# Performance work log

Measured on AMD Instinct MI355X. Metric: run time of the kernel, lower is better.

Reference implementation:

```python
import jax, jax.numpy as jnp
import numpy as np

B = 65536      # graphs per batch
NPG = 8        # nodes per graph (row_cluster has 8 entries)
N = B * NPG    # total nodes
P = 3 * B      # pooled nodes (3 row-clusters per graph)


def setup_inputs() -> dict:
    key = jax.random.key(0)
    ks = jax.random.split(key, 10)
    # per-graph edge template (undirected -> both directions); rows: {0,1,2},{3,4,5},{6,7}
    pairs = np.array([(0, 1), (1, 2), (0, 3), (3, 4), (4, 5), (3, 6), (6, 7), (2, 5), (5, 7), (1, 7)], dtype=np.int64)
    und = np.concatenate([pairs, pairs[:, ::-1]], axis=0)              # [20,2]
    off = (np.arange(B, dtype=np.int64) * NPG)[:, None, None]
    ei = (und[None] + off).reshape(-1, 2).T                            # [2, 20B]
    # pooled edges = avg_pool's coalesced cluster graph: triangle on 3 clusters per graph
    ppairs = np.array([(0, 1), (1, 2), (0, 2)], dtype=np.int64)
    pund = np.concatenate([ppairs, ppairs[:, ::-1]], axis=0)           # [6,2]
    poff = (np.arange(B, dtype=np.int64) * 3)[:, None, None]
    ei2 = (pund[None] + poff).reshape(-1, 2).T                         # [2, 6B]
    # consecutive-relabelled cluster assignment (PyG: 3*batch + [1,1,1,2,2,2,3,3] -> 0..3B-1)
    cluster = np.tile(np.array([0, 0, 0, 1, 1, 1, 2, 2], dtype=np.int64), B) + np.repeat(np.arange(B, dtype=np.int64) * 3, NPG)
    batch2 = np.arange(P, dtype=np.int64) // 3

    def lin(k, fan_in, fan_out):
        kw, kb = jax.random.split(k)
        s = 1.0 / np.sqrt(fan_in)
        W = jax.random.uniform(kw, (fan_in, fan_out), minval=-s, maxval=s, dtype=jnp.float32)
        b = jax.random.uniform(kb, (fan_out,), minval=-s, maxval=s, dtype=jnp.float32)
        return W, b

    W1, b1 = lin(ks[0], 336, 100)
    W2, b2 = lin(ks[1], 100, 100)
    W3, b3 = lin(ks[2], 100, 100)
    W4, b4 = lin(ks[3], 100, 100)
    W5, b5 = lin(ks[4], 100, 100)
    L1w, L1b = lin(ks[5], 100, 100)
    L2w, L2b = lin(ks[6], 100, 100)
    L3w, L3b = lin(ks[7], 100, 29)
    x = jax.random.normal(ks[8], (N, 336), dtype=jnp.float32)
    return dict(x=x, edge_index=jnp.asarray(ei), edge_index2=jnp.asarray(ei2),
                cluster=jnp.asarray(cluster), batch2=jnp.asarray(batch2),
                W1=W1, b1=b1, W2=W2, b2=b2, W3=W3, b3=b3, W4=W4, b4=b4, W5=W5, b5=b5,
                L1w=L1w, L1b=L1b, L2w=L2w, L2b=L2b, L3w=L3w, L3b=L3b)


def gcn(x, ei, W, b, n):
    # PyG GCNConv: x' = D^{-1/2}(A+I)D^{-1/2} (x W) + b
    h = x @ W
    loop = jnp.arange(n)
    s = jnp.concatenate([ei[0], loop])
    d = jnp.concatenate([ei[1], loop])
    deg = jax.ops.segment_sum(jnp.ones(s.shape[0], h.dtype), d, num_segments=n)
    dinv = jax.lax.rsqrt(deg)  # deg >= 1 because of self-loops
    norm = dinv[s] * dinv[d]
    return jax.ops.segment_sum(h[s] * norm[:, None], d, num_segments=n) + b


def reference(x, edge_index, edge_index2, cluster, batch2,
              W1, b1, W2, b2, W3, b3, W4, b4, W5, b5,
              L1w, L1b, L2w, L2b, L3w, L3b):
    h = jax.nn.relu(gcn(x, edge_index, W1, b1, N))
    h = jax.nn.relu(gcn(h, edge_index, W2, b2, N))
    h = jax.nn.relu(gcn(h, edge_index, W3, b3, N))
    # avg_pool: mean node features per cluster -> [P, 100]
    cnt = jax.ops.segment_sum(jnp.ones(N, h.dtype), cluster, num_segments=P)
    hp = jax.ops.segment_sum(h, cluster, num_segments=P) / cnt[:, None]
    hp = jax.nn.relu(gcn(hp, edge_index2, W4, b4, P))
    hp = jax.nn.relu(gcn(hp, edge_index2, W5, b5, P))
    # global_mean_pool over pooled-graph batch -> [B, 100]
    cnt2 = jax.ops.segment_sum(jnp.ones(P, hp.dtype), batch2, num_segments=B)
    g = jax.ops.segment_sum(hp, batch2, num_segments=B) / cnt2[:, None]
    g = jax.nn.relu(g @ L1w + L1b)
    g = jax.nn.relu(g @ L2w + L2b)
    return g @ L3w + L3b
```

## Files before the change

kernel.cpp:

```cpp
#include <hip/hip_runtime.h>


typedef __bf16 bf16_t;
typedef bf16_t bf16x8 __attribute__((ext_vector_type(8)));
typedef unsigned short u16x8 __attribute__((ext_vector_type(8)));
typedef float f32x4 __attribute__((ext_vector_type(4)));

#define C_ 0.28867513459481287f
#define T_ (1.0f/3.0f)
#define Q_ 0.25f

#define OFF_W1  0
#define OFF_W2  39424
#define OFF_W3  53760
#define OFF_W4  68096
#define OFF_W5  82432
#define OFF_L1W 96768
#define OFF_L2W 111104
#define OFF_L3W 125440
#define M_OFF_BYTES 262144

__device__ __forceinline__ unsigned short f2bf(float f) {
  return __builtin_bit_cast(unsigned short, (__bf16)f);
}
__device__ __forceinline__ float bf2f(unsigned short h) {
  unsigned u = ((unsigned)h) << 16;
  return __builtin_bit_cast(float, u);
}

__global__ __launch_bounds__(256) void prep_w(
    const float* __restrict__ W1, const float* __restrict__ W2,
    const float* __restrict__ W3, const float* __restrict__ W4,
    const float* __restrict__ W5, const float* __restrict__ L1w,
    const float* __restrict__ L2w, const float* __restrict__ L3w,
    unsigned short* __restrict__ ws)
{
  const int bid = blockIdx.x;
  int m, ct;
  if (bid < 7)       { m = 0; ct = bid; }
  else if (bid < 49) { m = 1 + (bid - 7) / 7; ct = (bid - 7) % 7; }
  else               { m = 7; ct = bid - 49; }
  const float* W; int K, NC, KSF; int off;
  switch (m) {
    case 0:  W = W1;  K = 336; NC = 100; KSF = 11; off = OFF_W1;  break;
    case 1:  W = W2;  K = 100; NC = 100; KSF = 4;  off = OFF_W2;  break;
    case 2:  W = W3;  K = 100; NC = 100; KSF = 4;  off = OFF_W3;  break;
    case 3:  W = W4;  K = 100; NC = 100; KSF = 4;  off = OFF_W4;  break;
    case 4:  W = W5;  K = 100; NC = 100; KSF = 4;  off = OFF_W5;  break;
    case 5:  W = L1w; K = 100; NC = 100; KSF = 4;  off = OFF_L1W; break;
    case 6:  W = L2w; K = 100; NC = 100; KSF = 4;  off = OFF_L2W; break;
    default: W = L3w; K = 100; NC = 29;  KSF = 4;  off = OFF_L3W; break;
  }
  for (int task = threadIdx.x; task < KSF * 64; task += 256) {
    const int ks = task >> 6, lane = task & 63;
    const int col = ct * 16 + (lane & 15);
    u16x8 o;
#pragma unroll
    for (int j = 0; j < 8; ++j) {
      const int k = ks * 32 + (lane >> 4) * 8 + j;
      const float v = (k < K && col < NC) ? W[(size_t)k * NC + col] : 0.f;
      o[j] = f2bf(v);
    }
    *(u16x8*)(ws + off + (size_t)(ct * KSF + ks) * 512 + (size_t)lane * 8) = o;
  }
}

#define MFMA1(ACC, AH, BH)                                                     \
  ACC = __builtin_amdgcn_mfma_f32_16x16x32_bf16(                               \
      __builtin_bit_cast(bf16x8, AH), __builtin_bit_cast(bf16x8, BH), ACC,     \
      0, 0, 0)

#define MFMA2S(ACC, AH, AL, BH)                                                \
  do {                                                                         \
    MFMA1(ACC, AH, BH);                                                        \
    MFMA1(ACC, AL, BH);                                                        \
  } while (0)

#define LOADB(MOFF, KSF_, CT, KS, BH)                                          \
  BH = *(const u16x8*)(ws + (MOFF) +                                           \
                       (size_t)((CT) * (KSF_) + (KS)) * 512 + lane8)

#define STORE_H(R, Cc, V)                                                      \
  do {                                                                         \
    const unsigned short hb_ = f2bf(V);                                        \
    const int pb_ = (R) * 256 + ((((Cc) * 2)) ^ (((R) & 7) << 4));             \
    *(unsigned short*)(Ahi + pb_) = hb_;                                       \
  } while (0)

#define DENSE_KLOOP(MOFF)                                                      \
  do {                                                                         \
    _Pragma("unroll")                                                          \
    for (int rt = 0; rt < 2; ++rt)                                             \
      _Pragma("unroll")                                                        \
      for (int ct = 0; ct < 7; ++ct) acc[rt][ct] = (f32x4){0.f, 0.f, 0.f, 0.f};\
    _Pragma("unroll 1")                                                        \
    for (int ks = 0; ks < 4; ++ks) {                                           \
      u16x8 ah[2];                                                             \
      _Pragma("unroll")                                                        \
      for (int rt = 0; rt < 2; ++rt) {                                         \
        const int row = w32 + rt * 16 + l15;                                   \
        const int pb = row * 256 + ((ks * 64 + q16) ^ ((row & 7) << 4));       \
        ah[rt] = *(const u16x8*)(Ahi + pb);                                    \
      }                                                                        \
      _Pragma("unroll")                                                        \
      for (int ct = 0; ct < 7; ++ct) {                                         \
        u16x8 bh;                                                              \
        LOADB(MOFF, 4, ct, ks, bh);                                            \
        MFMA1(acc[0][ct], ah[0], bh);                                          \
        MFMA1(acc[1][ct], ah[1], bh);                                          \
      }                                                                        \
    }                                                                          \
  } while (0)

#define EPI_MIX(BV)                                                            \
  do {                                                                         \
    _Pragma("unroll")                                                          \
    for (int rt = 0; rt < 2; ++rt) {                                           \
      _Pragma("unroll")                                                        \
      for (int ct = 0; ct < 7; ++ct) {                                         \
        const float v0 = acc[rt][ct][0], v1 = acc[rt][ct][1];                  \
        const float v2 = acc[rt][ct][2], v3 = acc[rt][ct][3];                  \
        const float u0 = __shfl_xor(v0, 16), u1 = __shfl_xor(v1, 16);          \
        const float u2 = __shfl_xor(v2, 16), u3 = __shfl_xor(v3, 16);          \
        float o0, o1, o2, o3;                                                  \
        if (!p1) {            \
          o0 = T_ * v0 + C_ * (v1 + v3);                                       \
          o1 = C_ * (v0 + v2) + Q_ * (v1 + u3);                                \
          o2 = T_ * v2 + C_ * (v1 + u1);                                       \
          o3 = Q_ * v3 + C_ * (v0 + u0 + u2);                                  \
        } else {              \
          o0 = T_ * v0 + C_ * (u3 + v1);                                       \
          o1 = Q_ * (v1 + v3) + C_ * (v0 + u2);                                \
          o2 = T_ * v2 + C_ * (u3 + v3);                                       \
          o3 = Q_ * (v3 + v1 + u1) + C_ * v2;                                  \
        }                                                                      \
        const int col = ct * 16 + l15;                                         \
        const float bv = BV[ct];                                               \
        float h0 = fmaxf(o0 + bv, 0.f), h1 = fmaxf(o1 + bv, 0.f);              \
        float h2 = fmaxf(o2 + bv, 0.f), h3 = fmaxf(o3 + bv, 0.f);              \
        if (col >= 100) { h0 = h1 = h2 = h3 = 0.f; }                           \
        const int rb = w32 + rt * 16 + 4 * q;                                  \
        STORE_H(rb + 0, col, h0); STORE_H(rb + 1, col, h1);                    \
        STORE_H(rb + 2, col, h2); STORE_H(rb + 3, col, h3);                    \
      }                                                                        \
    }                                                                          \
  } while (0)

__global__ __launch_bounds__(256, 3)
void rownet_node(const float* __restrict__ x,
                 const unsigned short* __restrict__ ws,
                 unsigned char* __restrict__ mws,
                 const float* __restrict__ b1, const float* __restrict__ b2,
                 const float* __restrict__ b3)
{
  __shared__ __align__(16) unsigned char smem[32768];
  unsigned char* const Ahi = smem;

  const int tid  = threadIdx.x;
  const int w    = tid >> 6;
  const int lane = tid & 63;
  const int l15  = lane & 15;
  const int q    = lane >> 4;
  const int q16  = q * 16;
  const int p1   = q & 1;
  const int lane8 = lane * 8;
  const int w32  = w * 32;
  const int g0   = blockIdx.x * 16;
  const int n0   = blockIdx.x * 128;

  float bv1[7], bv2[7], bv3[7];
#pragma unroll
  for (int ct = 0; ct < 7; ++ct) {
    const int col = ct * 16 + l15;
    const bool ok = (col < 100);
    bv1[ct] = ok ? b1[col] : 0.f;
    bv2[ct] = ok ? b2[col] : 0.f;
    bv3[ct] = ok ? b3[col] : 0.f;
  }

  f32x4 acc[2][7];

  {
    const float* const xb =
        x + (size_t)(n0 + w32 + l15) * 336 + q * 8;
    const bool qlow = (q < 2);
#pragma unroll
    for (int rt = 0; rt < 2; ++rt)
#pragma unroll
      for (int ct = 0; ct < 7; ++ct) acc[rt][ct] = (f32x4){0.f, 0.f, 0.f, 0.f};

#pragma unroll 1
    for (int ks = 0; ks < 11; ++ks) {
      u16x8 ah[2], al[2];
#pragma unroll
      for (int rt = 0; rt < 2; ++rt) {
        float4 p0, p1v;
        if (ks < 10 || qlow) {
          const float* xr = xb + (size_t)rt * (16 * 336) + ks * 32;
          p0  = *(const float4*)xr;
          p1v = *(const float4*)(xr + 4);
        } else {
          p0 = make_float4(0.f, 0.f, 0.f, 0.f);
          p1v = p0;
        }
        const float v[8] = {p0.x, p0.y, p0.z, p0.w, p1v.x, p1v.y, p1v.z, p1v.w};
#pragma unroll
        for (int j = 0; j < 8; ++j) {
          const unsigned short hb = f2bf(v[j]);
          ah[rt][j] = hb;
          al[rt][j] = f2bf(v[j] - bf2f(hb));
        }
      }
#pragma unroll
      for (int ct = 0; ct < 7; ++ct) {
        u16x8 bh;
        LOADB(OFF_W1, 11, ct, ks, bh);
#pragma unroll
        for (int rt = 0; rt < 2; ++rt)
          MFMA2S(acc[rt][ct], ah[rt], al[rt], bh);
      }
    }
  }
  {
    const int row = w32 + (lane & 31);
    const int half = lane >> 5;
    const int pb = row * 256 + ((224 + 16 * half) ^ ((row & 7) << 4));
    *(u16x8*)(Ahi + pb) = (u16x8){0, 0, 0, 0, 0, 0, 0, 0};
  }

  EPI_MIX(bv1);

  DENSE_KLOOP(OFF_W2);  EPI_MIX(bv2);
  DENSE_KLOOP(OFF_W3);

#pragma unroll
  for (int rt = 0; rt < 2; ++rt) {
#pragma unroll
    for (int ct = 0; ct < 7; ++ct) {
      const float v0 = acc[rt][ct][0], v1 = acc[rt][ct][1];
      const float v2 = acc[rt][ct][2], v3 = acc[rt][ct][3];
      const float u0 = __shfl_xor(v0, 16), u1 = __shfl_xor(v1, 16);
      const float u2 = __shfl_xor(v2, 16), u3 = __shfl_xor(v3, 16);
      float o0, o1, o2, o3;
      if (!p1) {
        o0 = T_ * v0 + C_ * (v1 + v3);
        o1 = C_ * (v0 + v2) + Q_ * (v1 + u3);
        o2 = T_ * v2 + C_ * (v1 + u1);
        o3 = Q_ * v3 + C_ * (v0 + u0 + u2);
      } else {
        o0 = T_ * v0 + C_ * (u3 + v1);
        o1 = Q_ * (v1 + v3) + C_ * (v0 + u2);
        o2 = T_ * v2 + C_ * (u3 + v3);
        o3 = Q_ * (v3 + v1 + u1) + C_ * v2;
      }
      const int col = ct * 16 + l15;
      const float bv = bv3[ct];
      float h0 = fmaxf(o0 + bv, 0.f), h1 = fmaxf(o1 + bv, 0.f);
      float h2 = fmaxf(o2 + bv, 0.f), h3 = fmaxf(o3 + bv, 0.f);
      if (col >= 100) { h0 = h1 = h2 = h3 = 0.f; }
      float pp = p1 ? ((h0 + h1) * (1.f/9.f) + (h2 + h3) * (1.f/6.f))
                    : ((h0 + h1 + h2 + h3) * (1.f/9.f));
      pp += __shfl_xor(pp, 16);
      if (!p1 && col < 100) {
        const int g_abs = g0 + 4 * w + 2 * rt + (q >> 1);
        const int blk2 = g_abs >> 7, r2 = g_abs & 127;
        const size_t byte = (size_t)blk2 * 32768 + r2 * 256
                          + ((col * 2) ^ ((r2 & 7) << 4));
        *(unsigned short*)(mws + byte) = f2bf(pp);
      }
    }
  }
}

#define EPI_PLAIN(BOFF)                                                        \
  do {                                                                         \
    _Pragma("unroll")                                                          \
    for (int rt = 0; rt < 2; ++rt) {                                           \
      _Pragma("unroll")                                                        \
      for (int ct = 0; ct < 7; ++ct) {                                         \
        const int col = ct * 16 + l15;                                         \
        const float bv = bs[(BOFF) + col];                                     \
        _Pragma("unroll")                                                      \
        for (int i = 0; i < 4; ++i) {                                          \
          float hv = fmaxf(acc[rt][ct][i] + bv, 0.f);                          \
          if (col >= 100) hv = 0.f;                                            \
          STORE_H(w32 + rt * 16 + 4 * q + i, col, hv);                         \
        }                                                                      \
      }                                                                        \
    }                                                                          \
  } while (0)

__global__ __launch_bounds__(256, 3)
void rownet_tail(const unsigned short* __restrict__ ws,
                 const unsigned char* __restrict__ mws,
                 const float* __restrict__ b4, const float* __restrict__ b5,
                 const float* __restrict__ L1b, const float* __restrict__ L2b,
                 const float* __restrict__ L3b,
                 float* __restrict__ out)
{
  __shared__ __align__(16) unsigned char smem[34496];
  unsigned char* const Ahi = smem;
  float* const bs = (float*)(smem + 32768);

  const int tid  = threadIdx.x;
  const int w    = tid >> 6;
  const int lane = tid & 63;
  const int l15  = lane & 15;
  const int q    = lane >> 4;
  const int q16  = q * 16;
  const int lane8 = lane * 8;
  const int w32  = w * 32;

  {
    const unsigned char* src = mws + (size_t)blockIdx.x * 32768;
#pragma unroll
    for (int it = 0; it < 8; ++it) {
      const int off = (it * 256 + tid) * 16;
      *(u16x8*)(Ahi + off) = *(const u16x8*)(src + off);
    }
  }
  if (tid < 100) {
    bs[      tid] = b4[tid];
    bs[100 + tid] = b5[tid];
    bs[200 + tid] = L1b[tid];
    bs[300 + tid] = L2b[tid];
  }
  if (tid < 29) bs[400 + tid] = L3b[tid];
  __syncthreads();

  f32x4 acc[2][7];
  DENSE_KLOOP(OFF_W4);  EPI_PLAIN(0);
  DENSE_KLOOP(OFF_W5);  EPI_PLAIN(100);
  DENSE_KLOOP(OFF_L1W); EPI_PLAIN(200);
  DENSE_KLOOP(OFF_L2W); EPI_PLAIN(300);

  {
    f32x4 c[2][2];
#pragma unroll
    for (int rt = 0; rt < 2; ++rt)
#pragma unroll
      for (int ct = 0; ct < 2; ++ct) c[rt][ct] = (f32x4){0.f, 0.f, 0.f, 0.f};
#pragma unroll
    for (int ks = 0; ks < 4; ++ks) {
      u16x8 ah[2];
#pragma unroll
      for (int rt = 0; rt < 2; ++rt) {
        const int row = w32 + rt * 16 + l15;
        const int pb = row * 256 + ((ks * 64 + q16) ^ ((row & 7) << 4));
        ah[rt] = *(const u16x8*)(Ahi + pb);
      }
#pragma unroll
      for (int ct = 0; ct < 2; ++ct) {
        u16x8 bh;
        LOADB(OFF_L3W, 4, ct, ks, bh);
        MFMA1(c[0][ct], ah[0], bh);
        MFMA1(c[1][ct], ah[1], bh);
      }
    }
    const size_t gbase = (size_t)blockIdx.x * 128;
#pragma unroll
    for (int rt = 0; rt < 2; ++rt)
#pragma unroll
      for (int ct = 0; ct < 2; ++ct) {
        const int col = ct * 16 + l15;
        if (col < 29) {
#pragma unroll
          for (int i = 0; i < 4; ++i) {
            const int row = w32 + rt * 16 + 4 * q + i;
            out[(gbase + row) * 29 + col] = c[rt][ct][i] + bs[400 + col];
          }
        }
      }
  }
}

extern "C" void kernel_launch(void* const* d_in, const int* in_sizes, int n_in,
                              void* d_out, int out_size, void* d_ws, size_t ws_size,
                              hipStream_t stream) {
  (void)in_sizes; (void)n_in; (void)out_size; (void)ws_size;
  const float* x   = (const float*)d_in[0];
  const float* W1  = (const float*)d_in[5];
  const float* b1  = (const float*)d_in[6];
  const float* W2  = (const float*)d_in[7];
  const float* b2  = (const float*)d_in[8];
  const float* W3  = (const float*)d_in[9];
  const float* b3  = (const float*)d_in[10];
  const float* W4  = (const float*)d_in[11];
  const float* b4  = (const float*)d_in[12];
  const float* W5  = (const float*)d_in[13];
  const float* b5  = (const float*)d_in[14];
  const float* L1w = (const float*)d_in[15];
  const float* L1b = (const float*)d_in[16];
  const float* L2w = (const float*)d_in[17];
  const float* L2b = (const float*)d_in[18];
  const float* L3w = (const float*)d_in[19];
  const float* L3b = (const float*)d_in[20];
  unsigned short* ws = (unsigned short*)d_ws;
  unsigned char* mws = (unsigned char*)d_ws + M_OFF_BYTES;

  prep_w<<<51, 256, 0, stream>>>(W1, W2, W3, W4, W5, L1w, L2w, L3w, ws);
  rownet_node<<<4096, 256, 0, stream>>>(x, ws, mws, b1, b2, b3);
  rownet_tail<<<512, 256, 0, stream>>>(ws, mws, b4, b5, L1b, L2b, L3b,
                                       (float*)d_out);
}
```

Measured before the change: 299.5 us.

## Process 64 rows per wave with 2-wave blocks in node kernel

The node kernel now runs 128-thread blocks where each wave handles 64 rows (4 row tiles) instead of 32, so each B-fragment load of the weights feeds four MFMAs instead of two. This halves weight-load traffic per MFMA and the number of waves per block. The cost is twice the accumulator registers (acc[4][7]) and a lower launch-bounds occupancy target, with fewer waves available to hide latency. The old 2-row-tile loop macro is kept for the tail kernel.

New measurement: 353.9 us. +18.2%, slower.

```diff
diff --git a/kernel.cpp b/kernel.cpp
--- a/kernel.cpp
+++ b/kernel.cpp
@@ -87,18 +87,18 @@
     *(unsigned short*)(Ahi + pb_) = hb_;                                       \
   } while (0)
 
-#define DENSE_KLOOP(MOFF)                                                      \
+#define DENSE_KLOOP4(MOFF)                                                     \
   do {                                                                         \
     _Pragma("unroll")                                                          \
-    for (int rt = 0; rt < 2; ++rt)                                             \
+    for (int rt = 0; rt < 4; ++rt)                                             \
       _Pragma("unroll")                                                        \
       for (int ct = 0; ct < 7; ++ct) acc[rt][ct] = (f32x4){0.f, 0.f, 0.f, 0.f};\
     _Pragma("unroll 1")                                                        \
     for (int ks = 0; ks < 4; ++ks) {                                           \
-      u16x8 ah[2];                                                             \
-      _Pragma("unroll")                                                        \
-      for (int rt = 0; rt < 2; ++rt) {                                         \
-        const int row = w32 + rt * 16 + l15;                                   \
+      u16x8 ah[4];                                                             \
+      _Pragma("unroll")                                                        \
+      for (int rt = 0; rt < 4; ++rt) {                                         \
+        const int row = w64 + rt * 16 + l15;                                   \
         const int pb = row * 256 + ((ks * 64 + q16) ^ ((row & 7) << 4));       \
         ah[rt] = *(const u16x8*)(Ahi + pb);                                    \
       }                                                                        \
@@ -108,14 +108,16 @@
         LOADB(MOFF, 4, ct, ks, bh);                                            \
         MFMA1(acc[0][ct], ah[0], bh);                                          \
         MFMA1(acc[1][ct], ah[1], bh);                                          \
+        MFMA1(acc[2][ct], ah[2], bh);                                          \
+        MFMA1(acc[3][ct], ah[3], bh);                                          \
       }                                                                        \
     }                                                                          \
   } while (0)
 
-#define EPI_MIX(BV)                                                            \
+#define EPI_MIX4(BV)                                                           \
   do {                                                                         \
     _Pragma("unroll")                                                          \
-    for (int rt = 0; rt < 2; ++rt) {                                           \
+    for (int rt = 0; rt < 4; ++rt) {                                           \
       _Pragma("unroll")                                                        \
       for (int ct = 0; ct < 7; ++ct) {                                         \
         const float v0 = acc[rt][ct][0], v1 = acc[rt][ct][1];                  \
@@ -139,14 +141,14 @@
         float h0 = fmaxf(o0 + bv, 0.f), h1 = fmaxf(o1 + bv, 0.f);              \
         float h2 = fmaxf(o2 + bv, 0.f), h3 = fmaxf(o3 + bv, 0.f);              \
         if (col >= 100) { h0 = h1 = h2 = h3 = 0.f; }                           \
-        const int rb = w32 + rt * 16 + 4 * q;                                  \
+        const int rb = w64 + rt * 16 + 4 * q;                                  \
         STORE_H(rb + 0, col, h0); STORE_H(rb + 1, col, h1);                    \
         STORE_H(rb + 2, col, h2); STORE_H(rb + 3, col, h3);                    \
       }                                                                        \
     }                                                                          \
   } while (0)
 
-__global__ __launch_bounds__(256, 3)
+__global__ __launch_bounds__(128, 2)
 void rownet_node(const float* __restrict__ x,
                  const unsigned short* __restrict__ ws,
                  unsigned char* __restrict__ mws,
@@ -164,7 +166,7 @@
   const int q16  = q * 16;
   const int p1   = q & 1;
   const int lane8 = lane * 8;
-  const int w32  = w * 32;
+  const int w64  = w * 64;
   const int g0   = blockIdx.x * 16;
   const int n0   = blockIdx.x * 128;
 
@@ -178,22 +180,22 @@
     bv3[ct] = ok ? b3[col] : 0.f;
   }
 
-  f32x4 acc[2][7];
+  f32x4 acc[4][7];
 
   {
     const float* const xb =
-        x + (size_t)(n0 + w32 + l15) * 336 + q * 8;
+        x + (size_t)(n0 + w64 + l15) * 336 + q * 8;
     const bool qlow = (q < 2);
 #pragma unroll
-    for (int rt = 0; rt < 2; ++rt)
+    for (int rt = 0; rt < 4; ++rt)
 #pragma unroll
       for (int ct = 0; ct < 7; ++ct) acc[rt][ct] = (f32x4){0.f, 0.f, 0.f, 0.f};
 
 #pragma unroll 1
     for (int ks = 0; ks < 11; ++ks) {
-      u16x8 ah[2], al[2];
-#pragma unroll
-      for (int rt = 0; rt < 2; ++rt) {
+      u16x8 ah[4], al[4];
+#pragma unroll
+      for (int rt = 0; rt < 4; ++rt) {
         float4 p0, p1v;
         if (ks < 10 || qlow) {
           const float* xr = xb + (size_t)rt * (16 * 336) + ks * 32;
@@ -216,25 +218,25 @@
         u16x8 bh;
         LOADB(OFF_W1, 11, ct, ks, bh);
 #pragma unroll
-        for (int rt = 0; rt < 2; ++rt)
+        for (int rt = 0; rt < 4; ++rt)
           MFMA2S(acc[rt][ct], ah[rt], al[rt], bh);
       }
     }
   }
-  {
-    const int row = w32 + (lane & 31);
-    const int half = lane >> 5;
-    const int pb = row * 256 + ((224 + 16 * half) ^ ((row & 7) << 4));
+#pragma unroll
+  for (int i = 0; i < 2; ++i) {
+    const int row = w64 + lane;
+    const int pb = row * 256 + ((224 + 16 * i) ^ ((row & 7) << 4));
     *(u16x8*)(Ahi + pb) = (u16x8){0, 0, 0, 0, 0, 0, 0, 0};
   }
 
-  EPI_MIX(bv1);
-
-  DENSE_KLOOP(OFF_W2);  EPI_MIX(bv2);
-  DENSE_KLOOP(OFF_W3);
-
-#pragma unroll
-  for (int rt = 0; rt < 2; ++rt) {
+  EPI_MIX4(bv1);
+
+  DENSE_KLOOP4(OFF_W2);  EPI_MIX4(bv2);
+  DENSE_KLOOP4(OFF_W3);
+
+#pragma unroll
+  for (int rt = 0; rt < 4; ++rt) {
 #pragma unroll
     for (int ct = 0; ct < 7; ++ct) {
       const float v0 = acc[rt][ct][0], v1 = acc[rt][ct][1];
@@ -262,7 +264,7 @@
                     : ((h0 + h1 + h2 + h3) * (1.f/9.f));
       pp += __shfl_xor(pp, 16);
       if (!p1 && col < 100) {
-        const int g_abs = g0 + 4 * w + 2 * rt + (q >> 1);
+        const int g_abs = g0 + 8 * w + 2 * rt + (q >> 1);
         const int blk2 = g_abs >> 7, r2 = g_abs & 127;
         const size_t byte = (size_t)blk2 * 32768 + r2 * 256
                           + ((col * 2) ^ ((r2 & 7) << 4));
@@ -271,6 +273,31 @@
     }
   }
 }
+
+#define DENSE_KLOOP(MOFF)                                                      \
+  do {                                                                         \
+    _Pragma("unroll")                                                          \
+    for (int rt = 0; rt < 2; ++rt)                                             \
+      _Pragma("unroll")                                                        \
+      for (int ct = 0; ct < 7; ++ct) acc[rt][ct] = (f32x4){0.f, 0.f, 0.f, 0.f};\
+    _Pragma("unroll 1")                                                        \
+    for (int ks = 0; ks < 4; ++ks) {                                           \
+      u16x8 ah[2];                                                             \
+      _Pragma("unroll")                                                        \
+      for (int rt = 0; rt < 2; ++rt) {                                         \
+        const int row = w32 + rt * 16 + l15;                                   \
+        const int pb = row * 256 + ((ks * 64 + q16) ^ ((row & 7) << 4));       \
+        ah[rt] = *(const u16x8*)(Ahi + pb);                                    \
+      }                                                                        \
+      _Pragma("unroll")                                                        \
+      for (int ct = 0; ct < 7; ++ct) {                                         \
+        u16x8 bh;                                                              \
+        LOADB(MOFF, 4, ct, ks, bh);                                            \
+        MFMA1(acc[0][ct], ah[0], bh);                                          \
+        MFMA1(acc[1][ct], ah[1], bh);                                          \
+      }                                                                        \
+    }                                                                          \
+  } while (0)
 
 #define EPI_PLAIN(BOFF)                                                        \
   do {                                                                         \
@@ -399,7 +426,7 @@
   unsigned char* mws = (unsigned char*)d_ws + M_OFF_BYTES;
 
   prep_w<<<51, 256, 0, stream>>>(W1, W2, W3, W4, W5, L1w, L2w, L3w, ws);
-  rownet_node<<<4096, 256, 0, stream>>>(x, ws, mws, b1, b2, b3);
+  rownet_node<<<4096, 128, 0, stream>>>(x, ws, mws, b1, b2, b3);
   rownet_tail<<<512, 256, 0, stream>>>(ws, mws, b4, b5, L1b, L2b, L3b,
                                        (float*)d_out);
 }
```
